# Kernel tuning notes

Measured on AMD Instinct MI355X. Metric: run time of the kernel, lower is better.

Reference implementation:

```python
import jax, jax.numpy as jnp
import numpy as np


def setup_inputs() -> dict:
    key = jax.random.key(0)
    k1, k2, k3, k4, k5 = jax.random.split(key, 5)
    B, C, H, W = 2, 3, 64, 64
    f_tar = jax.random.normal(k1, (B, C, H, W), dtype=jnp.float32)
    f_src = jax.random.normal(k2, (B, C, H, W), dtype=jnp.float32)
    # Pinhole intrinsics (focal=50, principal point at image center) + small noise,
    # guaranteed invertible.
    K_base = jnp.array([[50.0, 0.0, 32.0], [0.0, 50.0, 32.0], [0.0, 0.0, 1.0]],
                       dtype=jnp.float32)
    K = K_base[None] + 0.05 * jax.random.normal(k3, (B, 3, 3), dtype=jnp.float32)
    # Near-identity rotation-like matrix.
    R = jnp.eye(3, dtype=jnp.float32)[None] + 0.1 * jax.random.normal(
        k4, (B, 3, 3), dtype=jnp.float32)
    t = jax.random.normal(k5, (B, 3, 1), dtype=jnp.float32)
    return {"f_tar": f_tar, "f_src": f_src, "K": K, "R": R, "t": t}


def reference(f_tar, f_src, K, R, t):
    B, C, H, W = f_src.shape  # C == 3 (required by the cross product)
    N = H * W
    dtype = f_src.dtype

    f_src_flat = f_src.reshape(B, C, N)  # (B, 3, N)
    f_tar_flat = f_tar.reshape(B, C, N)  # (B, 3, N)

    # A[b, i, j] = <f_src[:, i], f_tar[:, j]>  -> (B, N, N)
    A = jnp.einsum('bci,bcj->bij', f_src_flat, f_tar_flat)

    # Homogeneous pixel coordinates (3, N): rows of meshgrid(H, W, indexing='ij').
    ix, iy = jnp.meshgrid(jnp.arange(H), jnp.arange(W), indexing='ij')
    pix = jnp.stack([ix.reshape(-1), iy.reshape(-1), jnp.ones(N, dtype=jnp.int32)],
                    axis=0).astype(dtype)  # (3, N)

    K_inv = jnp.linalg.inv(K)  # (B, 3, 3)
    # tar_proj = K @ (R @ (K^-1 @ x) + t)   -> (B, 3, N)
    cam_rays = jnp.einsum('bij,jn->bin', K_inv, pix)
    tar_proj = jnp.einsum('bij,bjn->bin', K, jnp.einsum('bij,bjn->bin', R, cam_rays) + t)
    # Origin projects to K @ (R @ 0 + t) = K @ t, broadcast over N.
    o_proj = jnp.einsum('bij,bjn->bin', K, t)  # (B, 3, 1)

    diff = tar_proj - o_proj  # (B, 3, N)

    # Epipolar distance: || (f_src - o) x diff || / ||diff||, broadcast to (B, N, N).
    a = f_src_flat[:, :, :, None] - o_proj[:, :, :, None]  # (B, 3, N, 1)
    b = diff[:, :, None, :]                                 # (B, 3, 1, N)
    cross = jnp.cross(a, b, axis=1)                         # (B, 3, N, N)
    cross_norm = jnp.linalg.norm(cross, axis=1)             # (B, N, N)
    diff_norm = jnp.linalg.norm(diff, axis=1, keepdims=True)  # (B, 1, N)
    d_epipolar = cross_norm / diff_norm                     # (B, N, N)

    # 'sigmoid' in the original is nn.Softmax(dim=-1).
    EPI_THRESH = 0.5
    SHARPNESS = 50.0
    weight_map = 1.0 - jax.nn.softmax(SHARPNESS * (d_epipolar - EPI_THRESH), axis=-1)

    A_weighted = A * weight_map
    attention_map = jax.nn.softmax(A_weighted, axis=1)  # normalize over src positions

    # (B, N, N) @ (B, N, C) -> (B, N, C), then raw view back to (B, C, H, W)
    attended = jnp.einsum('bik,bck->bic', attention_map, f_src_flat)
    return attended.reshape(B, C, H, W)
```

## Files before the change

### kernel.cpp

```cpp
#include <hip/hip_runtime.h>
#include <hip/hip_bf16.h>

namespace {
constexpr int BB = 2;
constexpr int NN = 4096;

constexpr int OFF_SRC4 = 0;
constexpr int OFF_TAR4 = 4 * BB * NN;
constexpr int OFF_U4   = 8 * BB * NN;
constexpr int OFF_W4   = 12 * BB * NN;
constexpr int OFF_ROW  = 16 * BB * NN;
constexpr int OFF_COL  = 18 * BB * NN;
constexpr int OFF_NMAX = 20 * BB * NN;
}

__device__ __forceinline__ float fsqrt(float x) { return __builtin_amdgcn_sqrtf(x); }

__global__ __launch_bounds__(256) void k_setup(
    const float* __restrict__ fsrc, const float* __restrict__ ftar,
    const float* __restrict__ Kb, const float* __restrict__ Rb,
    const float* __restrict__ tb, float* __restrict__ ws) {
  int gid = blockIdx.x * blockDim.x + threadIdx.x;
  if (gid >= BB * NN) return;
  int b = gid >> 12;
  int n = gid & (NN - 1);

  float K[9], R[9], t3[3];
#pragma unroll
  for (int k = 0; k < 9; k++) { K[k] = Kb[b * 9 + k]; R[k] = Rb[b * 9 + k]; }
#pragma unroll
  for (int k = 0; k < 3; k++) t3[k] = tb[b * 3 + k];

  float c00 = K[4] * K[8] - K[5] * K[7];
  float c01 = K[5] * K[6] - K[3] * K[8];
  float c02 = K[3] * K[7] - K[4] * K[6];
  float det = K[0] * c00 + K[1] * c01 + K[2] * c02;
  float id = 1.0f / det;
  float Ki[9];
  Ki[0] = c00 * id; Ki[1] = (K[2] * K[7] - K[1] * K[8]) * id; Ki[2] = (K[1] * K[5] - K[2] * K[4]) * id;
  Ki[3] = c01 * id; Ki[4] = (K[0] * K[8] - K[2] * K[6]) * id; Ki[5] = (K[2] * K[3] - K[0] * K[5]) * id;
  Ki[6] = c02 * id; Ki[7] = (K[1] * K[6] - K[0] * K[7]) * id; Ki[8] = (K[0] * K[4] - K[1] * K[3]) * id;

  float RK[9];
#pragma unroll
  for (int i = 0; i < 3; i++)
#pragma unroll
    for (int j = 0; j < 3; j++)
      RK[i * 3 + j] = R[i * 3 + 0] * Ki[j] + R[i * 3 + 1] * Ki[3 + j] + R[i * 3 + 2] * Ki[6 + j];
  float M3[9];
#pragma unroll
  for (int i = 0; i < 3; i++)
#pragma unroll
    for (int j = 0; j < 3; j++)
      M3[i * 3 + j] = K[i * 3 + 0] * RK[j] + K[i * 3 + 1] * RK[3 + j] + K[i * 3 + 2] * RK[6 + j];
  float o0 = K[0] * t3[0] + K[1] * t3[1] + K[2] * t3[2];
  float o1 = K[3] * t3[0] + K[4] * t3[1] + K[5] * t3[2];
  float o2 = K[6] * t3[0] + K[7] * t3[1] + K[8] * t3[2];

  float sx = fsrc[b * 3 * NN + 0 * NN + n];
  float sy = fsrc[b * 3 * NN + 1 * NN + n];
  float sz = fsrc[b * 3 * NN + 2 * NN + n];
  float tx = ftar[b * 3 * NN + 0 * NN + n];
  float ty = ftar[b * 3 * NN + 1 * NN + n];
  float tz = ftar[b * 3 * NN + 2 * NN + n];

  float ux = sx - o0, uy = sy - o1, uz = sz - o2;
  float usq = ux * ux + uy * uy + uz * uz;

  float px = (float)(n >> 6), py = (float)(n & 63);
  float vx = M3[0] * px + M3[1] * py + M3[2];
  float vy = M3[3] * px + M3[4] * py + M3[5];
  float vz = M3[6] * px + M3[7] * py + M3[8];
  float invn = rsqrtf(vx * vx + vy * vy + vz * vz);

  float4* src4 = (float4*)(ws + OFF_SRC4);
  float4* tar4 = (float4*)(ws + OFF_TAR4);
  float4* u4 = (float4*)(ws + OFF_U4);
  float4* w4 = (float4*)(ws + OFF_W4);
  src4[gid] = make_float4(sx, sy, sz, 0.f);
  tar4[gid] = make_float4(tx, ty, tz, 0.f);
  u4[gid] = make_float4(ux, uy, uz, usq);
  w4[gid] = make_float4(vx * invn, vy * invn, vz * invn, 0.f);

  float ns = fsqrt(sx * sx + sy * sy + sz * sz);
#pragma unroll
  for (int off = 32; off; off >>= 1) ns = fmaxf(ns, __shfl_xor(ns, off));
  if ((threadIdx.x & 63) == 0)
    atomicMax((unsigned int*)(ws + OFF_NMAX + b), __float_as_uint(ns));
}

__global__ __launch_bounds__(256, 4) void k_pass1(float* __restrict__ ws) {
  __shared__ float sred[4][8];
  const float4* u4 = (const float4*)(ws + OFF_U4);
  const float4* w4 = (const float4*)(ws + OFF_W4);
  float2* rowst = (float2*)(ws + OFF_ROW);
  int tid = threadIdx.x, wid = tid >> 6, lane = tid & 63;
  int g0 = blockIdx.x * 8;
  int b = g0 >> 12;

  float ux[8], uy[8], uz[8], us[8];
#pragma unroll
  for (int r = 0; r < 8; r++) {
    float4 u = u4[g0 + r];
    ux[r] = u.x; uy[r] = u.y; uz[r] = u.z; us[r] = u.w;
  }
  const float4* wb = w4 + b * NN;

  float mx[8] = {0.f, 0.f, 0.f, 0.f, 0.f, 0.f, 0.f, 0.f};
  for (int j = wid * 64 + lane; j < NN; j += 256) {
    float4 w = wb[j];
#pragma unroll
    for (int r = 0; r < 8; r++) {
      float dot = ux[r] * w.x + uy[r] * w.y + uz[r] * w.z;
      mx[r] = fmaxf(mx[r], us[r] - dot * dot);
    }
  }
#pragma unroll
  for (int off = 32; off; off >>= 1)
#pragma unroll
    for (int r = 0; r < 8; r++) mx[r] = fmaxf(mx[r], __shfl_xor(mx[r], off));
  if (lane == 0) {
#pragma unroll
    for (int r = 0; r < 8; r++) sred[wid][r] = mx[r];
  }
  __syncthreads();
  float m[8];
#pragma unroll
  for (int r = 0; r < 8; r++)
    m[r] = 50.f * fsqrt(fmaxf(fmaxf(sred[0][r], sred[1][r]), fmaxf(sred[2][r], sred[3][r])));
  __syncthreads();

  float s[8] = {0.f, 0.f, 0.f, 0.f, 0.f, 0.f, 0.f, 0.f};
  for (int j = wid * 64 + lane; j < NN; j += 256) {
    float4 w = wb[j];
#pragma unroll
    for (int r = 0; r < 8; r++) {
      float dot = ux[r] * w.x + uy[r] * w.y + uz[r] * w.z;
      float d2 = fmaxf(us[r] - dot * dot, 0.f);
      float t = 50.f * fsqrt(d2);
      s[r] += __expf(t - m[r]);
    }
  }
#pragma unroll
  for (int off = 32; off; off >>= 1)
#pragma unroll
    for (int r = 0; r < 8; r++) s[r] += __shfl_xor(s[r], off);
  if (lane == 0) {
#pragma unroll
    for (int r = 0; r < 8; r++) sred[wid][r] = s[r];
  }
  __syncthreads();
  if (tid < 8) {
    float tot = sred[0][tid] + sred[1][tid] + sred[2][tid] + sred[3][tid];
    rowst[g0 + tid] = make_float2(m[tid], 1.f / tot);
  }
}

__global__ __launch_bounds__(256, 4) void k_pass2(float* __restrict__ ws) {
  __shared__ float sred[4][8];
  const float4* u4 = (const float4*)(ws + OFF_U4);
  const float4* w4 = (const float4*)(ws + OFF_W4);
  const float4* src4 = (const float4*)(ws + OFF_SRC4);
  const float4* tar4 = (const float4*)(ws + OFF_TAR4);
  const float2* rowst = (const float2*)(ws + OFF_ROW);
  float2* colst = (float2*)(ws + OFF_COL);
  int tid = threadIdx.x, wid = tid >> 6, lane = tid & 63;
  int c0 = blockIdx.x * 8;
  int b = c0 >> 12;
  int base = b * NN;
  float maxns = ws[OFF_NMAX + b];

  float wx[8], wy[8], wz[8], tx[8], ty[8], tz[8], Mb[8];
#pragma unroll
  for (int r = 0; r < 8; r++) {
    float4 w = w4[c0 + r];
    float4 tt = tar4[c0 + r];
    wx[r] = w.x; wy[r] = w.y; wz[r] = w.z;
    tx[r] = tt.x; ty[r] = tt.y; tz[r] = tt.z;
    Mb[r] = maxns * fsqrt(tt.x * tt.x + tt.y * tt.y + tt.z * tt.z);
  }

  float S[8] = {0.f, 0.f, 0.f, 0.f, 0.f, 0.f, 0.f, 0.f};
  for (int i = wid * 64 + lane; i < NN; i += 256) {
    float4 u = u4[base + i];
    float4 sv = src4[base + i];
    float2 rs = rowst[base + i];
#pragma unroll
    for (int r = 0; r < 8; r++) {
      float dot = u.x * wx[r] + u.y * wy[r] + u.z * wz[r];
      float d2 = fmaxf(u.w - dot * dot, 0.f);
      float t = 50.f * fsqrt(d2);
      float e = __expf(t - rs.x);
      float wgt = 1.f - e * rs.y;
      float A = sv.x * tx[r] + sv.y * ty[r] + sv.z * tz[r];
      S[r] += __expf(A * wgt - Mb[r]);
    }
  }
#pragma unroll
  for (int off = 32; off; off >>= 1)
#pragma unroll
    for (int r = 0; r < 8; r++) S[r] += __shfl_xor(S[r], off);
  if (lane == 0) {
#pragma unroll
    for (int r = 0; r < 8; r++) sred[wid][r] = S[r];
  }
  __syncthreads();
  if (tid < 8) {
    float tot = sred[0][tid] + sred[1][tid] + sred[2][tid] + sred[3][tid];
    colst[c0 + tid] = make_float2(Mb[tid], 1.f / tot);
  }
}

__global__ __launch_bounds__(256, 4) void k_pass3(const float* __restrict__ ws,
                                                  float* __restrict__ out) {
  __shared__ float sacc[4][24];
  const float4* u4 = (const float4*)(ws + OFF_U4);
  const float4* w4 = (const float4*)(ws + OFF_W4);
  const float4* src4 = (const float4*)(ws + OFF_SRC4);
  const float4* tar4 = (const float4*)(ws + OFF_TAR4);
  const float2* rowst = (const float2*)(ws + OFF_ROW);
  const float2* colst = (const float2*)(ws + OFF_COL);
  int tid = threadIdx.x, wid = tid >> 6, lane = tid & 63;
  int g0 = blockIdx.x * 8;
  int b = g0 >> 12;
  int base = b * NN;

  float ux[8], uy[8], uz[8], us[8], mrow[8], invden[8], sx[8], sy[8], sz[8];
#pragma unroll
  for (int r = 0; r < 8; r++) {
    float4 u = u4[g0 + r];
    float2 rs = rowst[g0 + r];
    float4 sv = src4[g0 + r];
    ux[r] = u.x; uy[r] = u.y; uz[r] = u.z; us[r] = u.w;
    mrow[r] = rs.x; invden[r] = rs.y;
    sx[r] = sv.x; sy[r] = sv.y; sz[r] = sv.z;
  }
  float acc[8][3];
#pragma unroll
  for (int r = 0; r < 8; r++) { acc[r][0] = 0.f; acc[r][1] = 0.f; acc[r][2] = 0.f; }

  for (int j = wid * 64 + lane; j < NN; j += 256) {
    float4 w = w4[base + j];
    float4 tt = tar4[base + j];
    float4 sj = src4[base + j];
    float2 cs = colst[base + j];
#pragma unroll
    for (int r = 0; r < 8; r++) {
      float dot = ux[r] * w.x + uy[r] * w.y + uz[r] * w.z;
      float d2 = fmaxf(us[r] - dot * dot, 0.f);
      float t = 50.f * fsqrt(d2);
      float e = __expf(t - mrow[r]);
      float wgt = 1.f - e * invden[r];
      float A = sx[r] * tt.x + sy[r] * tt.y + sz[r] * tt.z;
      float p = __expf(A * wgt - cs.x) * cs.y;
      acc[r][0] += p * sj.x;
      acc[r][1] += p * sj.y;
      acc[r][2] += p * sj.z;
    }
  }
#pragma unroll
  for (int off = 32; off; off >>= 1)
#pragma unroll
    for (int r = 0; r < 8; r++) {
      acc[r][0] += __shfl_xor(acc[r][0], off);
      acc[r][1] += __shfl_xor(acc[r][1], off);
      acc[r][2] += __shfl_xor(acc[r][2], off);
    }
  if (lane == 0) {
#pragma unroll
    for (int r = 0; r < 8; r++) {
      sacc[wid][r * 3 + 0] = acc[r][0];
      sacc[wid][r * 3 + 1] = acc[r][1];
      sacc[wid][r * 3 + 2] = acc[r][2];
    }
  }
  __syncthreads();
  if (tid < 24) {
    float v = sacc[0][tid] + sacc[1][tid] + sacc[2][tid] + sacc[3][tid];
    out[g0 * 3 + tid] = v;
  }
}

extern "C" void kernel_launch(void* const* d_in, const int* in_sizes, int n_in,
                              void* d_out, int out_size, void* d_ws, size_t ws_size,
                              hipStream_t stream) {
  (void)in_sizes; (void)n_in; (void)out_size; (void)ws_size;
  const float* ftar = (const float*)d_in[0];
  const float* fsrc = (const float*)d_in[1];
  const float* K = (const float*)d_in[2];
  const float* R = (const float*)d_in[3];
  const float* t = (const float*)d_in[4];
  float* ws = (float*)d_ws;
  float* out = (float*)d_out;

  hipMemsetAsync((char*)d_ws + OFF_NMAX * sizeof(float), 0, BB * sizeof(float), stream);

  k_setup<<<dim3((BB * NN + 255) / 256), dim3(256), 0, stream>>>(fsrc, ftar, K, R, t, ws);
  k_pass1<<<dim3(1024), dim3(256), 0, stream>>>(ws);
  k_pass2<<<dim3(1024), dim3(256), 0, stream>>>(ws);
  k_pass3<<<dim3(1024), dim3(256), 0, stream>>>(ws, out);
}
```

Measured before the change: 134.6 us.

## Materialize fp16 exponent matrices between passes instead of recomputing

Pass 1 now writes the per-pair epipolar softmax exponentials to an fp16 N×N workspace buffer. Pass 2 reads that buffer to form the column-softmax exponentials, stores them as a second fp16 matrix, and accumulates column sums with atomics. Pass 3 then only reads those stored exponentials and does the weighted sum, rather than recomputing sqrt and exp. This trades repeated transcendental math for about 128 MB of extra memory traffic, lowers precision to fp16, and replaces the fixed per-column max with a bias constant, which risks overflow or underflow.

```diff
diff --git a/kernel.cpp b/kernel.cpp
--- a/kernel.cpp
+++ b/kernel.cpp
@@ -9,12 +9,20 @@
 constexpr int OFF_TAR4 = 4 * BB * NN;
 constexpr int OFF_U4   = 8 * BB * NN;
 constexpr int OFF_W4   = 12 * BB * NN;
-constexpr int OFF_ROW  = 16 * BB * NN;
-constexpr int OFF_COL  = 18 * BB * NN;
-constexpr int OFF_NMAX = 20 * BB * NN;
+constexpr int OFF_RINV = 16 * BB * NN;
+constexpr int OFF_CS   = 17 * BB * NN;
+constexpr int OFF_NMAX = 18 * BB * NN;
+constexpr size_t OFF_E1B = (size_t)1 << 20;
+constexpr size_t NHALF   = (size_t)BB * NN * NN;
+constexpr size_t OFF_E2B = OFF_E1B + NHALF * 2;
+constexpr float L2E = 1.4426950408889634f;
+constexpr float S50 = 72.13475204444817f;
+constexpr float BIAS = 10.0f;
 }
 
 __device__ __forceinline__ float fsqrt(float x) { return __builtin_amdgcn_sqrtf(x); }
+__device__ __forceinline__ float ex2(float x) { return __builtin_amdgcn_exp2f(x); }
+__device__ __forceinline__ float frcp(float x) { return __builtin_amdgcn_rcpf(x); }
 
 __global__ __launch_bounds__(256) void k_setup(
     const float* __restrict__ fsrc, const float* __restrict__ ftar,
@@ -93,7 +101,8 @@
   __shared__ float sred[4][8];
   const float4* u4 = (const float4*)(ws + OFF_U4);
   const float4* w4 = (const float4*)(ws + OFF_W4);
-  float2* rowst = (float2*)(ws + OFF_ROW);
+  float* rinv = ws + OFF_RINV;
+  _Float16* eh = (_Float16*)((char*)ws + OFF_E1B);
   int tid = threadIdx.x, wid = tid >> 6, lane = tid & 63;
   int g0 = blockIdx.x * 8;
   int b = g0 >> 12;
@@ -124,10 +133,10 @@
     for (int r = 0; r < 8; r++) sred[wid][r] = mx[r];
   }
   __syncthreads();
-  float m[8];
+  float m2[8];
 #pragma unroll
   for (int r = 0; r < 8; r++)
-    m[r] = 50.f * fsqrt(fmaxf(fmaxf(sred[0][r], sred[1][r]), fmaxf(sred[2][r], sred[3][r])));
+    m2[r] = S50 * fsqrt(fmaxf(fmaxf(sred[0][r], sred[1][r]), fmaxf(sred[2][r], sred[3][r])));
   __syncthreads();
 
   float s[8] = {0.f, 0.f, 0.f, 0.f, 0.f, 0.f, 0.f, 0.f};
@@ -137,8 +146,10 @@
     for (int r = 0; r < 8; r++) {
       float dot = ux[r] * w.x + uy[r] * w.y + uz[r] * w.z;
       float d2 = fmaxf(us[r] - dot * dot, 0.f);
-      float t = 50.f * fsqrt(d2);
-      s[r] += __expf(t - m[r]);
+      float t = fsqrt(d2);
+      float ev = ex2(fmaf(S50, t, -m2[r]));
+      s[r] += ev;
+      eh[(size_t)(g0 + r) * NN + j] = (_Float16)ev;
     }
   }
 #pragma unroll
@@ -152,107 +163,77 @@
   __syncthreads();
   if (tid < 8) {
     float tot = sred[0][tid] + sred[1][tid] + sred[2][tid] + sred[3][tid];
-    rowst[g0 + tid] = make_float2(m[tid], 1.f / tot);
-  }
-}
-
-__global__ __launch_bounds__(256, 4) void k_pass2(float* __restrict__ ws) {
-  __shared__ float sred[4][8];
-  const float4* u4 = (const float4*)(ws + OFF_U4);
-  const float4* w4 = (const float4*)(ws + OFF_W4);
+    rinv[g0 + tid] = 1.f / tot;
+  }
+}
+
+__global__ __launch_bounds__(256, 8) void k_pass2(float* __restrict__ ws) {
+  __shared__ float sS[4][64];
   const float4* src4 = (const float4*)(ws + OFF_SRC4);
   const float4* tar4 = (const float4*)(ws + OFF_TAR4);
-  const float2* rowst = (const float2*)(ws + OFF_ROW);
-  float2* colst = (float2*)(ws + OFF_COL);
+  const float* rinv = ws + OFF_RINV;
+  float* CS = ws + OFF_CS;
+  const _Float16* eh = (const _Float16*)((char*)ws + OFF_E1B);
+  _Float16* Eh = (_Float16*)((char*)ws + OFF_E2B);
+
   int tid = threadIdx.x, wid = tid >> 6, lane = tid & 63;
-  int c0 = blockIdx.x * 8;
-  int b = c0 >> 12;
+  int g = blockIdx.x >> 4;
+  int c = blockIdx.x & 15;
+  int gc = g * 64 + lane;
+  int b = gc >> 12;
   int base = b * NN;
+  int jloc = gc - base;
   float maxns = ws[OFF_NMAX + b];
 
-  float wx[8], wy[8], wz[8], tx[8], ty[8], tz[8], Mb[8];
-#pragma unroll
-  for (int r = 0; r < 8; r++) {
-    float4 w = w4[c0 + r];
-    float4 tt = tar4[c0 + r];
-    wx[r] = w.x; wy[r] = w.y; wz[r] = w.z;
-    tx[r] = tt.x; ty[r] = tt.y; tz[r] = tt.z;
-    Mb[r] = maxns * fsqrt(tt.x * tt.x + tt.y * tt.y + tt.z * tt.z);
-  }
-
-  float S[8] = {0.f, 0.f, 0.f, 0.f, 0.f, 0.f, 0.f, 0.f};
-  for (int i = wid * 64 + lane; i < NN; i += 256) {
-    float4 u = u4[base + i];
+  float4 tt = tar4[gc];
+  float Cj = BIAS - maxns * L2E * fsqrt(tt.x * tt.x + tt.y * tt.y + tt.z * tt.z);
+  float txl = tt.x * L2E, tyl = tt.y * L2E, tzl = tt.z * L2E;
+
+  float S = 0.f;
+  int i0 = c * 256 + wid * 64;
+#pragma unroll 4
+  for (int it = 0; it < 64; ++it) {
+    int i = i0 + it;
     float4 sv = src4[base + i];
-    float2 rs = rowst[base + i];
-#pragma unroll
-    for (int r = 0; r < 8; r++) {
-      float dot = u.x * wx[r] + u.y * wy[r] + u.z * wz[r];
-      float d2 = fmaxf(u.w - dot * dot, 0.f);
-      float t = 50.f * fsqrt(d2);
-      float e = __expf(t - rs.x);
-      float wgt = 1.f - e * rs.y;
-      float A = sv.x * tx[r] + sv.y * ty[r] + sv.z * tz[r];
-      S[r] += __expf(A * wgt - Mb[r]);
-    }
-  }
-#pragma unroll
-  for (int off = 32; off; off >>= 1)
-#pragma unroll
-    for (int r = 0; r < 8; r++) S[r] += __shfl_xor(S[r], off);
-  if (lane == 0) {
-#pragma unroll
-    for (int r = 0; r < 8; r++) sred[wid][r] = S[r];
-  }
-  __syncthreads();
-  if (tid < 8) {
-    float tot = sred[0][tid] + sred[1][tid] + sred[2][tid] + sred[3][tid];
-    colst[c0 + tid] = make_float2(Mb[tid], 1.f / tot);
-  }
-}
-
-__global__ __launch_bounds__(256, 4) void k_pass3(const float* __restrict__ ws,
+    float invd = rinv[base + i];
+    float ev = (float)eh[(size_t)(base + i) * NN + jloc];
+    float wgt = fmaf(-ev, invd, 1.f);
+    float Ap = sv.x * txl + sv.y * tyl + sv.z * tzl;
+    float Ev = ex2(fmaf(Ap, wgt, Cj));
+    S += Ev;
+    Eh[(size_t)(base + i) * NN + jloc] = (_Float16)Ev;
+  }
+  sS[wid][lane] = S;
+  __syncthreads();
+  if (wid == 0) {
+    float tot = sS[0][lane] + sS[1][lane] + sS[2][lane] + sS[3][lane];
+    atomicAdd(&CS[gc], tot);
+  }
+}
+
+__global__ __launch_bounds__(256, 8) void k_pass3(const float* __restrict__ ws,
                                                   float* __restrict__ out) {
-  __shared__ float sacc[4][24];
-  const float4* u4 = (const float4*)(ws + OFF_U4);
-  const float4* w4 = (const float4*)(ws + OFF_W4);
+  __shared__ float sacc[4][12];
   const float4* src4 = (const float4*)(ws + OFF_SRC4);
-  const float4* tar4 = (const float4*)(ws + OFF_TAR4);
-  const float2* rowst = (const float2*)(ws + OFF_ROW);
-  const float2* colst = (const float2*)(ws + OFF_COL);
+  const float* CS = ws + OFF_CS;
+  const _Float16* Eh = (const _Float16*)((const char*)ws + OFF_E2B);
   int tid = threadIdx.x, wid = tid >> 6, lane = tid & 63;
-  int g0 = blockIdx.x * 8;
+  int g0 = blockIdx.x * 4;
   int b = g0 >> 12;
   int base = b * NN;
 
-  float ux[8], uy[8], uz[8], us[8], mrow[8], invden[8], sx[8], sy[8], sz[8];
-#pragma unroll
-  for (int r = 0; r < 8; r++) {
-    float4 u = u4[g0 + r];
-    float2 rs = rowst[g0 + r];
-    float4 sv = src4[g0 + r];
-    ux[r] = u.x; uy[r] = u.y; uz[r] = u.z; us[r] = u.w;
-    mrow[r] = rs.x; invden[r] = rs.y;
-    sx[r] = sv.x; sy[r] = sv.y; sz[r] = sv.z;
-  }
-  float acc[8][3];
-#pragma unroll
-  for (int r = 0; r < 8; r++) { acc[r][0] = 0.f; acc[r][1] = 0.f; acc[r][2] = 0.f; }
-
+  float acc[4][3];
+#pragma unroll
+  for (int r = 0; r < 4; r++) { acc[r][0] = 0.f; acc[r][1] = 0.f; acc[r][2] = 0.f; }
+
+#pragma unroll 2
   for (int j = wid * 64 + lane; j < NN; j += 256) {
-    float4 w = w4[base + j];
-    float4 tt = tar4[base + j];
     float4 sj = src4[base + j];
-    float2 cs = colst[base + j];
-#pragma unroll
-    for (int r = 0; r < 8; r++) {
-      float dot = ux[r] * w.x + uy[r] * w.y + uz[r] * w.z;
-      float d2 = fmaxf(us[r] - dot * dot, 0.f);
-      float t = 50.f * fsqrt(d2);
-      float e = __expf(t - mrow[r]);
-      float wgt = 1.f - e * invden[r];
-      float A = sx[r] * tt.x + sy[r] * tt.y + sz[r] * tt.z;
-      float p = __expf(A * wgt - cs.x) * cs.y;
+    float invS = frcp(CS[base + j]);
+#pragma unroll
+    for (int r = 0; r < 4; r++) {
+      float Ev = (float)Eh[(size_t)(g0 + r) * NN + j];
+      float p = Ev * invS;
       acc[r][0] += p * sj.x;
       acc[r][1] += p * sj.y;
       acc[r][2] += p * sj.z;
@@ -261,21 +242,21 @@
 #pragma unroll
   for (int off = 32; off; off >>= 1)
 #pragma unroll
-    for (int r = 0; r < 8; r++) {
+    for (int r = 0; r < 4; r++) {
       acc[r][0] += __shfl_xor(acc[r][0], off);
       acc[r][1] += __shfl_xor(acc[r][1], off);
       acc[r][2] += __shfl_xor(acc[r][2], off);
     }
   if (lane == 0) {
 #pragma unroll
-    for (int r = 0; r < 8; r++) {
+    for (int r = 0; r < 4; r++) {
       sacc[wid][r * 3 + 0] = acc[r][0];
       sacc[wid][r * 3 + 1] = acc[r][1];
       sacc[wid][r * 3 + 2] = acc[r][2];
     }
   }
   __syncthreads();
-  if (tid < 24) {
+  if (tid < 12) {
     float v = sacc[0][tid] + sacc[1][tid] + sacc[2][tid] + sacc[3][tid];
     out[g0 * 3 + tid] = v;
   }
@@ -293,10 +274,11 @@
   float* ws = (float*)d_ws;
   float* out = (float*)d_out;
 
-  hipMemsetAsync((char*)d_ws + OFF_NMAX * sizeof(float), 0, BB * sizeof(float), stream);
+  hipMemsetAsync((char*)d_ws + (size_t)OFF_CS * sizeof(float), 0,
+                 (size_t)(BB * NN + BB) * sizeof(float), stream);
 
   k_setup<<<dim3((BB * NN + 255) / 256), dim3(256), 0, stream>>>(fsrc, ftar, K, R, t, ws);
   k_pass1<<<dim3(1024), dim3(256), 0, stream>>>(ws);
-  k_pass2<<<dim3(1024), dim3(256), 0, stream>>>(ws);
-  k_pass3<<<dim3(1024), dim3(256), 0, stream>>>(ws, out);
-}
+  k_pass2<<<dim3(2048), dim3(256), 0, stream>>>(ws);
+  k_pass3<<<dim3(2048), dim3(256), 0, stream>>>(ws, out);
+}
```

Measured after the change: 142.9 us. 6.2% more time.
